# Performance work log

Measured on AMD Instinct MI355X. Metric: run time of the kernel, lower is better.

The kernel has to match this reference:

```python
import jax, jax.numpy as jnp
import numpy as np

C_IN, C_OUT, K, DG, PAD = 256, 256, 3, 2, 1
EPS = 1e-5


def setup_inputs() -> dict:
    key = jax.random.key(0)
    k = jax.random.split(key, 8)
    B, H, W = 4, 64, 64
    x = jax.random.normal(k[0], (B, C_IN, H, W), jnp.float32)
    # offset/mask conv (DCNv2 pack): 3 * dg * k * k output channels
    w_off = jax.random.normal(k[1], (3 * DG * K * K, C_IN, K, K), jnp.float32) * 0.01
    b_off = jnp.zeros((3 * DG * K * K,), jnp.float32)
    # main deformable conv weight
    w = jax.random.normal(k[2], (C_OUT, C_IN, K, K), jnp.float32) * (1.0 / np.sqrt(C_IN * K * K))
    b = jnp.zeros((C_OUT,), jnp.float32)
    # BatchNorm (eval mode: running stats)
    gamma = jnp.ones((C_OUT,), jnp.float32)
    beta = jnp.zeros((C_OUT,), jnp.float32)
    running_mean = jax.random.normal(k[3], (C_OUT,), jnp.float32) * 0.1
    running_var = jax.random.uniform(k[4], (C_OUT,), jnp.float32, 0.5, 1.5)
    return dict(x=x, w_off=w_off, b_off=b_off, w=w, b=b, gamma=gamma, beta=beta,
                running_mean=running_mean, running_var=running_var)


def _conv2d_same(x, w, b):
    y = jax.lax.conv_general_dilated(x, w, (1, 1), 'SAME',
                                     dimension_numbers=('NCHW', 'OIHW', 'NCHW'))
    return y + b[None, :, None, None]


def _deform_conv(x, w_off, b_off, w, b):
    B, C, H, W = x.shape
    K2 = K * K
    Cg = C // DG
    # offsets + modulation mask from internal conv (DCNv2 pack)
    om = _conv2d_same(x, w_off, b_off)            # [B, 3*DG*K2, H, W]
    o1, o2, m = jnp.split(om, 3, axis=1)
    mask = jax.nn.sigmoid(m).reshape(B, DG, 1, K2, H * W)
    off_y = o1.reshape(B, DG, K2, H, W)
    off_x = o2.reshape(B, DG, K2, H, W)
    # base sampling grid: output pixel + kernel tap - pad
    ki = jnp.arange(K)
    ky = (jnp.repeat(ki, K) - PAD).astype(jnp.float32)   # [K2]
    kx = (jnp.tile(ki, K) - PAD).astype(jnp.float32)     # [K2]
    py = off_y + ky[:, None, None] + jnp.arange(H, dtype=jnp.float32)[None, :, None]
    px = off_x + kx[:, None, None] + jnp.arange(W, dtype=jnp.float32)[None, None, :]
    y0 = jnp.floor(py)
    x0 = jnp.floor(px)
    ly = (py - y0).reshape(B, DG, 1, K2, H * W)
    lx = (px - x0).reshape(B, DG, 1, K2, H * W)
    y0i = y0.astype(jnp.int32)
    x0i = x0.astype(jnp.int32)
    xg = x.reshape(B, DG, Cg, H * W)

    def gather(yi, xi):
        # zero-padded bilinear corner gather, per deformable group
        valid = (yi >= 0) & (yi < H) & (xi >= 0) & (xi < W)
        lin = jnp.clip(yi, 0, H - 1) * W + jnp.clip(xi, 0, W - 1)
        v = jnp.take_along_axis(xg[:, :, :, None, :],
                                lin.reshape(B, DG, 1, K2, H * W), axis=-1)
        return v * valid.reshape(B, DG, 1, K2, H * W)

    val = (gather(y0i, x0i) * (1 - ly) * (1 - lx)
           + gather(y0i, x0i + 1) * (1 - ly) * lx
           + gather(y0i + 1, x0i) * ly * (1 - lx)
           + gather(y0i + 1, x0i + 1) * ly * lx)
    val = val * mask                               # [B, DG, Cg, K2, H*W]
    wr = w.reshape(C_OUT, DG, Cg, K2)
    out = jnp.einsum('bgckn,ogck->bon', val, wr).reshape(B, C_OUT, H, W)
    return out + b[None, :, None, None]


def reference(x, w_off, b_off, w, b, gamma, beta, running_mean, running_var):
    y = _deform_conv(x, w_off, b_off, w, b)
    inv = gamma / jnp.sqrt(running_var + EPS)
    y = (y - running_mean[None, :, None, None]) * inv[None, :, None, None] + beta[None, :, None, None]
    return jax.nn.relu(y)
```

## Files before the change

### kernel.cpp

```cpp
#include <hip/hip_runtime.h>
#include <math.h>

typedef __bf16 bf16x8 __attribute__((ext_vector_type(8)));
typedef float  f32x4  __attribute__((ext_vector_type(4)));
typedef int    i32x4  __attribute__((ext_vector_type(4)));

#define MFMA16(a, b, c) __builtin_amdgcn_mfma_f32_16x16x32_bf16((a), (b), (c), 0, 0, 0)

#define ATIDX(r, c) ((r) * 128 + (((c) ^ ((r) & 7)) * 8))

__global__ __launch_bounds__(256) void setup_kernel(
    const float* __restrict__ x, const float* __restrict__ w,
    const float* __restrict__ w_off, const float* __restrict__ bconv,
    const float* __restrict__ gamma, const float* __restrict__ beta,
    const float* __restrict__ mean, const float* __restrict__ var,
    __bf16* __restrict__ xT, __bf16* __restrict__ wFragD,
    __bf16* __restrict__ wFragO, float* __restrict__ sc,
    float* __restrict__ sh) {
  int t = threadIdx.x;
  if (blockIdx.x < 1024) {
    __shared__ float xs[64][65];
    int b = blockIdx.x >> 8, y = (blockIdx.x >> 2) & 63, cc = blockIdx.x & 3;
    const float* xb = x + (((size_t)b * 256 + cc * 64) * 64 + y) * 64;
    #pragma unroll
    for (int r = 0; r < 4; ++r) {
      int cl = r * 16 + (t >> 4), xc = (t & 15) * 4;
      f32x4 v = *(const f32x4*)(xb + (size_t)cl * 4096 + xc);
      xs[cl][xc] = v.x; xs[cl][xc + 1] = v.y;
      xs[cl][xc + 2] = v.z; xs[cl][xc + 3] = v.w;
    }
    __syncthreads();
    __bf16* dst = xT + (((size_t)b * 64 + y) * 64) * 256 + cc * 64;
    #pragma unroll
    for (int it = 0; it < 2; ++it) {
      int w2 = t + it * 256;
      int xc = w2 >> 3, cl8 = (w2 & 7) * 8;
      bf16x8 o;
      #pragma unroll
      for (int e = 0; e < 8; ++e) o[e] = (__bf16)xs[cl8 + e][xc];
      *(bf16x8*)(dst + (size_t)xc * 256 + cl8) = o;
    }
    return;
  }
  if (blockIdx.x < 1312) {
    int u = (blockIdx.x - 1024) * 256 + t;
    int lane = u & 63, ocb = (u >> 6) & 15, kc = (u >> 10) & 3, gk = u >> 12;
    int oc = ocb * 16 + (lane & 15);
    int cb = kc * 32 + (lane >> 4) * 8;
    int g = gk / 9, ktap = gk % 9;
    const float* src = w + ((size_t)oc * 256 + g * 128 + cb) * 9 + ktap;
    bf16x8 o;
    #pragma unroll
    for (int j = 0; j < 8; ++j) o[j] = (__bf16)src[(size_t)j * 9];
    *(bf16x8*)(wFragD + (size_t)u * 8) = o;
    return;
  }
  if (blockIdx.x < 1384) {
    int u = (blockIdx.x - 1312) * 256 + t;
    int lane = u & 63, ocq = (u >> 6) & 3, kc = (u >> 8) & 7, tap = u >> 11;
    int oc = ocq * 16 + (lane & 15);
    int cb = kc * 32 + (lane >> 4) * 8;
    bf16x8 o;
    #pragma unroll
    for (int j = 0; j < 8; ++j) o[j] = (__bf16)0.f;
    if (oc < 54) {
      const float* src = w_off + ((size_t)oc * 256 + cb) * 9 + tap;
      #pragma unroll
      for (int j = 0; j < 8; ++j) o[j] = (__bf16)src[(size_t)j * 9];
    }
    *(bf16x8*)(wFragO + (size_t)u * 8) = o;
    return;
  }
  if (t < 256) {
    float s = gamma[t] * rsqrtf(var[t] + 1e-5f);
    sc[t] = s;
    sh[t] = (bconv[t] - mean[t]) * s + beta[t];
  }
}

struct PhaseC {
  f32x4 swgtv[18 * 64];
  i32x4 slinv[18 * 64];
  __bf16 atile[2][2][64 * 128];
};
union FusedLDS {
  __bf16 rowbuf[3 * 66 * 256];
  PhaseC c;
};

__global__ __launch_bounds__(1024, 4) void fused_kernel(
    const __bf16* __restrict__ xT, const __bf16* __restrict__ wFragD,
    const __bf16* __restrict__ wFragO, const float* __restrict__ b_off,
    const float* __restrict__ sc, const float* __restrict__ sh,
    float* __restrict__ out) {
  __shared__ __attribute__((aligned(16))) FusedLDS U;
  __shared__ float omrow[2][54 * 64];
  int t = threadIdx.x;
  int b = blockIdx.x >> 6, y = blockIdx.x & 63;
  int lane = t & 63, wv = t >> 6;
  int l15 = lane & 15, quad = lane >> 4;
  const __bf16* xTb = xT + (size_t)b * 64 * 64 * 256;
  bf16x8 z8;
  #pragma unroll
  for (int e = 0; e < 8; ++e) z8[e] = (__bf16)0.f;

  for (int i = t; i < 3 * 66 * 32; i += 1024) {
    int c = i & 31, px66 = (i >> 5) % 66, dy = i / 2112;
    int y2 = y + dy - 1, x2 = px66 - 1;
    bf16x8 v = z8;
    if (y2 >= 0 && y2 < 64 && x2 >= 0 && x2 < 64)
      v = *(const bf16x8*)(xTb + ((size_t)y2 * 64 + x2) * 256 + c * 8);
    *(bf16x8*)&U.rowbuf[dy * 16896 + px66 * 256 + ((c ^ (px66 & 7)) * 8)] = v;
  }
  __syncthreads();

  {
    int kh = wv & 1, pxt = (wv >> 1) & 3, ocd = wv >> 3;
    f32x4 acc0 = {0.f, 0.f, 0.f, 0.f};
    f32x4 acc1 = {0.f, 0.f, 0.f, 0.f};
    for (int tap = 0; tap < 9; ++tap) {
      int dy = tap / 3, dxs = tap % 3;
      const __bf16* bb =
          wFragO + ((size_t)(tap * 8 + kh * 4) * 4 + ocd * 2) * 512 + lane * 8;
      bf16x8 Bf0[4], Bf1[4];
      #pragma unroll
      for (int kcl = 0; kcl < 4; ++kcl) {
        Bf0[kcl] = *(const bf16x8*)(bb + (size_t)kcl * 4 * 512);
        Bf1[kcl] = *(const bf16x8*)(bb + (size_t)kcl * 4 * 512 + 512);
      }
      int p0 = pxt * 16 + l15 + dxs;
      const __bf16* rb = U.rowbuf + dy * 16896;
      #pragma unroll
      for (int kcl = 0; kcl < 4; ++kcl) {
        int c = (kh * 4 + kcl) * 4 + quad;
        bf16x8 a0 = *(const bf16x8*)&rb[p0 * 256 + ((c ^ (p0 & 7)) * 8)];
        acc0 = MFMA16(a0, Bf0[kcl], acc0);
        acc1 = MFMA16(a0, Bf1[kcl], acc1);
      }
    }
    #pragma unroll
    for (int fo = 0; fo < 2; ++fo) {
      f32x4 v = fo ? acc1 : acc0;
      int oc = (ocd * 2 + fo) * 16 + l15;
      if (oc < 54)
        *(f32x4*)&omrow[kh][oc * 64 + pxt * 16 + quad * 4] = v;
    }
  }
  __syncthreads();

  for (int i = t; i < 18 * 64; i += 1024) {
    int gk = i >> 6, pb = i & 63;
    int k = gk % 9;
    float oy = omrow[0][gk * 64 + pb] + omrow[1][gk * 64 + pb] + b_off[gk];
    float ox = omrow[0][(18 + gk) * 64 + pb] + omrow[1][(18 + gk) * 64 + pb]
             + b_off[18 + gk];
    float mz = omrow[0][(36 + gk) * 64 + pb] + omrow[1][(36 + gk) * 64 + pb]
             + b_off[36 + gk];
    float mv = 1.f / (1.f + expf(-mz));
    float py  = (float)(y + (k / 3) - 1) + oy;
    float pxf = (float)(pb + (k % 3) - 1) + ox;
    float y0f = floorf(py), x0f = floorf(pxf);
    int y0 = (int)y0f, x0 = (int)x0f;
    float ly = py - y0f, lx = pxf - x0f;
    int y1 = y0 + 1, x1 = x0 + 1;
    bool vy0 = (y0 >= 0) && (y0 < 64), vy1 = (y1 >= 0) && (y1 < 64);
    bool vx0 = (x0 >= 0) && (x0 < 64), vx1 = (x1 >= 0) && (x1 < 64);
    int cy0 = min(max(y0, 0), 63), cy1 = min(max(y1, 0), 63);
    int cx0 = min(max(x0, 0), 63), cx1 = min(max(x1, 0), 63);
    f32x4 sv;
    sv.x = (vy0 && vx0) ? (1.f - ly) * (1.f - lx) * mv : 0.f;
    sv.y = (vy0 && vx1) ? (1.f - ly) * lx * mv : 0.f;
    sv.z = (vy1 && vx0) ? ly * (1.f - lx) * mv : 0.f;
    sv.w = (vy1 && vx1) ? ly * lx * mv : 0.f;
    i32x4 lv;
    lv.x = (cy0 * 64 + cx0) * 256;
    lv.y = (cy0 * 64 + cx1) * 256;
    lv.z = (cy1 * 64 + cx0) * 256;
    lv.w = (cy1 * 64 + cx1) * 256;
    U.c.swgtv[i] = sv;
    U.c.slinv[i] = lv;
  }

  f32x4 acc[4];
  #pragma unroll
  for (int fm = 0; fm < 4; ++fm) acc[fm] = (f32x4){0.f, 0.f, 0.f, 0.f};

  __syncthreads();

  int ch0 = l15 * 8;
  int p = wv * 4 + quad;
  #pragma unroll
  for (int t2 = 0; t2 < 2; ++t2) {
    const __bf16* xg = xTb + ch0;
    f32x4 sv = U.c.swgtv[t2 * 64 + p];
    i32x4 lv = U.c.slinv[t2 * 64 + p];
    bf16x8 c0 = *(const bf16x8*)(xg + lv.x);
    bf16x8 c1 = *(const bf16x8*)(xg + lv.y);
    bf16x8 c2 = *(const bf16x8*)(xg + lv.z);
    bf16x8 c3 = *(const bf16x8*)(xg + lv.w);
    bf16x8 o;
    #pragma unroll
    for (int e = 0; e < 8; ++e)
      o[e] = (__bf16)(sv.x * (float)c0[e] + sv.y * (float)c1[e]
                    + sv.z * (float)c2[e] + sv.w * (float)c3[e]);
    *(bf16x8*)&U.c.atile[0][t2][ATIDX(p, l15)] = o;
  }

  for (int iv = 0; iv < 9; ++iv) {
    __syncthreads();
    bf16x8 Bf0[4], Bf1[4];
    {
      const __bf16* bb0 =
          wFragD + ((size_t)(2 * iv) * 4 * 16 + wv) * 512 + lane * 8;
      const __bf16* bb1 = bb0 + (size_t)4 * 16 * 512;
      #pragma unroll
      for (int kc = 0; kc < 4; ++kc)
        Bf0[kc] = *(const bf16x8*)(bb0 + (size_t)kc * 16 * 512);
      #pragma unroll
      for (int kc = 0; kc < 4; ++kc)
        Bf1[kc] = *(const bf16x8*)(bb1 + (size_t)kc * 16 * 512);
    }
    bf16x8 cr[2][4];
    f32x4 sv[2];
    if (iv < 8) {
      #pragma unroll
      for (int t2 = 0; t2 < 2; ++t2) {
        int gn = 2 * iv + 2 + t2;
        const __bf16* xg = xTb + (gn / 9) * 128 + ch0;
        sv[t2] = U.c.swgtv[gn * 64 + p];
        i32x4 lv = U.c.slinv[gn * 64 + p];
        cr[t2][0] = *(const bf16x8*)(xg + lv.x);
        cr[t2][1] = *(const bf16x8*)(xg + lv.y);
        cr[t2][2] = *(const bf16x8*)(xg + lv.z);
        cr[t2][3] = *(const bf16x8*)(xg + lv.w);
      }
    }
    __builtin_amdgcn_sched_barrier(0);
    {
      const __bf16* at0 = U.c.atile[iv & 1][0];
      #pragma unroll
      for (int kc = 0; kc < 4; ++kc) {
        #pragma unroll
        for (int fm = 0; fm < 4; ++fm) {
          bf16x8 a = *(const bf16x8*)&at0[ATIDX(fm * 16 + l15, kc * 4 + quad)];
          acc[fm] = MFMA16(a, Bf0[kc], acc[fm]);
        }
      }
      const __bf16* at1 = U.c.atile[iv & 1][1];
      #pragma unroll
      for (int kc = 0; kc < 4; ++kc) {
        #pragma unroll
        for (int fm = 0; fm < 4; ++fm) {
          bf16x8 a = *(const bf16x8*)&at1[ATIDX(fm * 16 + l15, kc * 4 + quad)];
          acc[fm] = MFMA16(a, Bf1[kc], acc[fm]);
        }
      }
    }
    __builtin_amdgcn_sched_barrier(0);
    if (iv < 8) {
      #pragma unroll
      for (int t2 = 0; t2 < 2; ++t2) {
        __bf16* dst = U.c.atile[(iv + 1) & 1][t2];
        bf16x8 o;
        #pragma unroll
        for (int e = 0; e < 8; ++e)
          o[e] = (__bf16)(sv[t2].x * (float)cr[t2][0][e]
                        + sv[t2].y * (float)cr[t2][1][e]
                        + sv[t2].z * (float)cr[t2][2][e]
                        + sv[t2].w * (float)cr[t2][3][e]);
        *(bf16x8*)&dst[ATIDX(p, l15)] = o;
      }
    }
  }

  {
    int oc = wv * 16 + l15;
    float s = sc[oc], h = sh[oc];
    #pragma unroll
    for (int fm = 0; fm < 4; ++fm) {
      f32x4 v = acc[fm];
      f32x4 r = {fmaxf(v.x * s + h, 0.f), fmaxf(v.y * s + h, 0.f),
                 fmaxf(v.z * s + h, 0.f), fmaxf(v.w * s + h, 0.f)};
      int pxs = fm * 16 + quad * 4;
      *(f32x4*)(out + (((size_t)b * 256 + oc) * 64 + y) * 64 + pxs) = r;
    }
  }
}

extern "C" void kernel_launch(void* const* d_in, const int* in_sizes, int n_in,
                              void* d_out, int out_size, void* d_ws, size_t ws_size,
                              hipStream_t stream) {
  const float* x     = (const float*)d_in[0];
  const float* w_off = (const float*)d_in[1];
  const float* b_off = (const float*)d_in[2];
  const float* w     = (const float*)d_in[3];
  const float* bconv = (const float*)d_in[4];
  const float* gamma = (const float*)d_in[5];
  const float* beta  = (const float*)d_in[6];
  const float* rmean = (const float*)d_in[7];
  const float* rvar  = (const float*)d_in[8];
  float* out = (float*)d_out;

  __bf16* xT     = (__bf16*)d_ws;
  __bf16* wFragD = (__bf16*)((char*)d_ws + 8388608);
  __bf16* wFragO = (__bf16*)((char*)d_ws + 9568256);
  float*  sc     = (float*)((char*)d_ws + 9863168);
  float*  sh     = (float*)((char*)d_ws + 9864192);

  setup_kernel<<<1385, 256, 0, stream>>>(
      x, w, w_off, bconv, gamma, beta, rmean, rvar, xT, wFragD, wFragO, sc, sh);
  fused_kernel<<<4 * 64, 1024, 0, stream>>>(xT, wFragD, wFragO, b_off, sc, sh, out);
}
```

Measured before the change: 130.6 us.

## Split-K across wave halves with two output tiles per wave in deform GEMM

Each wave now computes two 16-channel output tiles over half of each K chunk, not one tile over the full K. This reuses every LDS A-fragment read for two MFMAs, halving A-tile LDS traffic per MFMA, and halves per-wave B-fragment register loads. The two K halves are summed through an LDS reduction before the BN/ReLU epilogue, which adds extra barriers and LDS writes. The accumulator registers double, and the launch_bounds minimum-blocks hint is dropped to leave room for them.

Result: slower. 136.9 us (+4.8%).

```diff
diff --git a/kernel.cpp b/kernel.cpp
--- a/kernel.cpp
+++ b/kernel.cpp
@@ -88,7 +88,7 @@
   PhaseC c;
 };
 
-__global__ __launch_bounds__(1024, 4) void fused_kernel(
+__global__ __launch_bounds__(1024) void fused_kernel(
     const __bf16* __restrict__ xT, const __bf16* __restrict__ wFragD,
     const __bf16* __restrict__ wFragO, const float* __restrict__ b_off,
     const float* __restrict__ sc, const float* __restrict__ sh,
@@ -181,9 +181,13 @@
     U.c.slinv[i] = lv;
   }
 
-  f32x4 acc[4];
+  int ocp = wv & 7, kh = wv >> 3;
+  f32x4 acc[4][2];
   #pragma unroll
-  for (int fm = 0; fm < 4; ++fm) acc[fm] = (f32x4){0.f, 0.f, 0.f, 0.f};
+  for (int fm = 0; fm < 4; ++fm)
+    #pragma unroll
+    for (int fn = 0; fn < 2; ++fn)
+      acc[fm][fn] = (f32x4){0.f, 0.f, 0.f, 0.f};
 
   __syncthreads();
 
@@ -208,17 +212,17 @@
 
   for (int iv = 0; iv < 9; ++iv) {
     __syncthreads();
-    bf16x8 Bf0[4], Bf1[4];
+    bf16x8 Bf[2][2][2];
     {
-      const __bf16* bb0 =
-          wFragD + ((size_t)(2 * iv) * 4 * 16 + wv) * 512 + lane * 8;
-      const __bf16* bb1 = bb0 + (size_t)4 * 16 * 512;
-      #pragma unroll
-      for (int kc = 0; kc < 4; ++kc)
-        Bf0[kc] = *(const bf16x8*)(bb0 + (size_t)kc * 16 * 512);
-      #pragma unroll
-      for (int kc = 0; kc < 4; ++kc)
-        Bf1[kc] = *(const bf16x8*)(bb1 + (size_t)kc * 16 * 512);
+      #pragma unroll
+      for (int t2 = 0; t2 < 2; ++t2)
+        #pragma unroll
+        for (int kc2 = 0; kc2 < 2; ++kc2)
+          #pragma unroll
+          for (int fn = 0; fn < 2; ++fn)
+            Bf[t2][kc2][fn] = *(const bf16x8*)(
+                wFragD + ((size_t)((2 * iv + t2) * 4 + kh * 2 + kc2) * 16
+                          + ocp * 2 + fn) * 512 + lane * 8);
     }
     bf16x8 cr[2][4];
     f32x4 sv[2];
@@ -237,22 +241,18 @@
     }
     __builtin_amdgcn_sched_barrier(0);
     {
-      const __bf16* at0 = U.c.atile[iv & 1][0];
-      #pragma unroll
-      for (int kc = 0; kc < 4; ++kc) {
+      #pragma unroll
+      for (int t2 = 0; t2 < 2; ++t2) {
+        const __bf16* at = U.c.atile[iv & 1][t2];
         #pragma unroll
-        for (int fm = 0; fm < 4; ++fm) {
-          bf16x8 a = *(const bf16x8*)&at0[ATIDX(fm * 16 + l15, kc * 4 + quad)];
-          acc[fm] = MFMA16(a, Bf0[kc], acc[fm]);
-        }
-      }
-      const __bf16* at1 = U.c.atile[iv & 1][1];
-      #pragma unroll
-      for (int kc = 0; kc < 4; ++kc) {
-        #pragma unroll
-        for (int fm = 0; fm < 4; ++fm) {
-          bf16x8 a = *(const bf16x8*)&at1[ATIDX(fm * 16 + l15, kc * 4 + quad)];
-          acc[fm] = MFMA16(a, Bf1[kc], acc[fm]);
+        for (int kc2 = 0; kc2 < 2; ++kc2) {
+          #pragma unroll
+          for (int fm = 0; fm < 4; ++fm) {
+            bf16x8 a = *(const bf16x8*)
+                &at[ATIDX(fm * 16 + l15, (kh * 2 + kc2) * 4 + quad)];
+            acc[fm][0] = MFMA16(a, Bf[t2][kc2][0], acc[fm][0]);
+            acc[fm][1] = MFMA16(a, Bf[t2][kc2][1], acc[fm][1]);
+          }
         }
       }
     }
@@ -273,16 +273,34 @@
     }
   }
 
-  {
-    int oc = wv * 16 + l15;
-    float s = sc[oc], h = sh[oc];
+  __syncthreads();
+  float* red = (float*)U.c.atile[0][0];
+  if (kh == 1) {
+    #pragma unroll
+    for (int fm = 0; fm < 4; ++fm)
+      #pragma unroll
+      for (int fn = 0; fn < 2; ++fn)
+        *(f32x4*)&red[(((ocp * 4 + fm) * 2 + fn) * 64 + lane) * 4] =
+            acc[fm][fn];
+  }
+  __syncthreads();
+  if (kh == 0) {
     #pragma unroll
     for (int fm = 0; fm < 4; ++fm) {
-      f32x4 v = acc[fm];
-      f32x4 r = {fmaxf(v.x * s + h, 0.f), fmaxf(v.y * s + h, 0.f),
-                 fmaxf(v.z * s + h, 0.f), fmaxf(v.w * s + h, 0.f)};
-      int pxs = fm * 16 + quad * 4;
-      *(f32x4*)(out + (((size_t)b * 256 + oc) * 64 + y) * 64 + pxs) = r;
+      #pragma unroll
+      for (int fn = 0; fn < 2; ++fn) {
+        f32x4 pv = *(const f32x4*)&red[(((ocp * 4 + fm) * 2 + fn) * 64
+                                        + lane) * 4];
+        int oc = ocp * 32 + fn * 16 + l15;
+        float s = sc[oc], h = sh[oc];
+        f32x4 v = acc[fm][fn];
+        f32x4 r = {fmaxf((v.x + pv.x) * s + h, 0.f),
+                   fmaxf((v.y + pv.y) * s + h, 0.f),
+                   fmaxf((v.z + pv.z) * s + h, 0.f),
+                   fmaxf((v.w + pv.w) * s + h, 0.f)};
+        int pxs = fm * 16 + quad * 4;
+        *(f32x4*)(out + (((size_t)b * 256 + oc) * 64 + y) * 64 + pxs) = r;
+      }
     }
   }
 }
```
